# Kernel tuning notes

Measured on AMD Instinct MI355X. Metric: run time of the kernel, lower is better.

## Reference

```python
import jax, jax.numpy as jnp
import numpy as np

WS = (2, 7, 7)       # window size (d,h,w)
SS = (1, 3, 3)       # shift size
NH = 6               # num heads
EPS = 1e-5


def _layernorm(x, g, b):
    m = jnp.mean(x, axis=-1, keepdims=True)
    v = jnp.mean((x - m) ** 2, axis=-1, keepdims=True)
    return (x - m) * jax.lax.rsqrt(v + EPS) * g + b


def _window_partition(x, ws):
    # x: (B, D, H, W, C) -> (B*nW, N, C)
    B, D, H, W, C = x.shape
    x = x.reshape(B, D // ws[0], ws[0], H // ws[1], ws[1], W // ws[2], ws[2], C)
    x = x.transpose(0, 1, 3, 5, 2, 4, 6, 7)
    return x.reshape(-1, ws[0] * ws[1] * ws[2], C)


def _window_reverse(w, ws, B, D, H, W):
    # w: (B*nW, N, C) -> (B, D, H, W, C)
    C = w.shape[-1]
    x = w.reshape(B, D // ws[0], H // ws[1], W // ws[2], ws[0], ws[1], ws[2], C)
    x = x.transpose(0, 1, 4, 2, 5, 3, 6, 7)
    return x.reshape(B, D, H, W, C)


def _rel_pos_index(ws):
    coords = np.stack(np.meshgrid(np.arange(ws[0]), np.arange(ws[1]), np.arange(ws[2]), indexing='ij'))
    cf = coords.reshape(3, -1)                      # (3, N)
    rel = cf[:, :, None] - cf[:, None, :]           # (3, N, N)
    rel = rel.transpose(1, 2, 0).copy()             # (N, N, 3)
    rel[..., 0] += ws[0] - 1
    rel[..., 1] += ws[1] - 1
    rel[..., 2] += ws[2] - 1
    rel[..., 0] *= (2 * ws[1] - 1) * (2 * ws[2] - 1)
    rel[..., 1] *= 2 * ws[2] - 1
    return rel.sum(-1)                              # (N, N) int


def _compute_mask(Dp, Hp, Wp, ws, ss):
    img = np.zeros((1, Dp, Hp, Wp, 1), np.float32)
    cnt = 0
    for d in (slice(-ws[0]), slice(-ws[0], -ss[0]), slice(-ss[0], None)):
        for h in (slice(-ws[1]), slice(-ws[1], -ss[1]), slice(-ss[1], None)):
            for w in (slice(-ws[2]), slice(-ws[2], -ss[2]), slice(-ss[2], None)):
                img[:, d, h, w, :] = cnt
                cnt += 1
    mw = np.asarray(_window_partition(jnp.asarray(img), ws)).squeeze(-1)  # (nW, N)
    am = mw[:, None, :] - mw[:, :, None]
    return np.where(am != 0, -100.0, 0.0).astype(np.float32)


def setup_inputs() -> dict:
    key = jax.random.key(0)
    ks = jax.random.split(key, 8)
    B, D, H, W, C = 4, 8, 56, 56, 192
    hid = 4 * C
    tbl = (2 * WS[0] - 1) * (2 * WS[1] - 1) * (2 * WS[2] - 1)
    s = 0.02
    return {
        'x': jax.random.normal(ks[0], (B, D, H, W, C), jnp.float32),
        'mask_matrix': jnp.asarray(_compute_mask(D, H, W, WS, SS)),
        'norm1_g': jnp.ones((C,), jnp.float32),
        'norm1_b': jnp.zeros((C,), jnp.float32),
        'qkv_w': jax.random.normal(ks[1], (3 * C, C), jnp.float32) * s,
        'qkv_b': jnp.zeros((3 * C,), jnp.float32),
        'rpb_table': jax.random.normal(ks[2], (tbl, NH), jnp.float32) * s,
        'proj_w': jax.random.normal(ks[3], (C, C), jnp.float32) * s,
        'proj_b': jnp.zeros((C,), jnp.float32),
        'norm2_g': jnp.ones((C,), jnp.float32),
        'norm2_b': jnp.zeros((C,), jnp.float32),
        'fc1_w': jax.random.normal(ks[4], (hid, C), jnp.float32) * s,
        'fc1_b': jnp.zeros((hid,), jnp.float32),
        'fc2_w': jax.random.normal(ks[5], (C, hid), jnp.float32) * s,
        'fc2_b': jnp.zeros((C,), jnp.float32),
    }


def reference(x, mask_matrix, norm1_g, norm1_b, qkv_w, qkv_b, rpb_table,
              proj_w, proj_b, norm2_g, norm2_b, fc1_w, fc1_b, fc2_w, fc2_b):
    B, D, H, W, C = x.shape
    hd = C // NH
    scale = hd ** -0.5
    N = WS[0] * WS[1] * WS[2]
    rpi = _rel_pos_index(WS)  # constant (N, N)

    shortcut = x
    h = _layernorm(x, norm1_g, norm1_b)
    # cyclic shift (dims divisible by window, no padding needed)
    sx = jnp.roll(h, (-SS[0], -SS[1], -SS[2]), axis=(1, 2, 3))
    xw = _window_partition(sx, WS)                      # (B_, N, C)
    B_ = xw.shape[0]

    qkv = (xw @ qkv_w.T + qkv_b).reshape(B_, N, 3, NH, hd).transpose(2, 0, 3, 1, 4)
    q, k, v = qkv[0] * scale, qkv[1], qkv[2]            # (B_, NH, N, hd)
    attn = jnp.einsum('bhnd,bhmd->bhnm', q, k)          # (B_, NH, N, N)

    bias = rpb_table[rpi.reshape(-1)].reshape(N, N, NH).transpose(2, 0, 1)
    attn = attn + bias[None]

    nW = mask_matrix.shape[0]
    attn = attn.reshape(B_ // nW, nW, NH, N, N) + mask_matrix[None, :, None]
    attn = jax.nn.softmax(attn.reshape(B_, NH, N, N), axis=-1)

    out = jnp.einsum('bhnm,bhmd->bhnd', attn, v).swapaxes(1, 2).reshape(B_, N, C)
    out = out @ proj_w.T + proj_b

    sx = _window_reverse(out, WS, B, D, H, W)
    x1 = jnp.roll(sx, (SS[0], SS[1], SS[2]), axis=(1, 2, 3))

    x = shortcut + x1
    h2 = _layernorm(x, norm2_g, norm2_b)
    h2 = jax.nn.gelu(h2 @ fc1_w.T + fc1_b, approximate=False) @ fc2_w.T + fc2_b
    return x + h2
```

## Files before the change

kernel.cpp:

```cpp
#include <hip/hip_runtime.h>
#include <math.h>

typedef short short8 __attribute__((ext_vector_type(8)));
typedef __bf16 bf16x8 __attribute__((ext_vector_type(8)));
typedef float floatx4 __attribute__((ext_vector_type(4)));
typedef float f32x4 __attribute__((ext_vector_type(4)));
typedef unsigned short ushort;
typedef unsigned int uint;

#define NTOK 100352
#define CCH 192
#define NWIN 1024
#define NSEQ 98
#define NSEQP 112
#define NHEAD 6
#define HD 32
#define VSTR 136
#define PSTR 40

typedef const __attribute__((address_space(1))) uint guint_t;
typedef __attribute__((address_space(3))) uint luint_t;

__device__ __forceinline__ float bf2f(ushort u) {
    union { uint i; float f; } x; x.i = ((uint)u) << 16; return x.f;
}
__device__ __forceinline__ ushort f2bf(float f) {
    uint u = __float_as_uint(f);
    uint r = (u + 0x7FFFu + ((u >> 16) & 1u)) >> 16;
    return (ushort)r;
}
__device__ __forceinline__ uint pack2bf(float a, float b) {
    return (uint)f2bf(a) | ((uint)f2bf(b) << 16);
}
__device__ __forceinline__ float ldT(const void* p, size_t i, bool bf) {
    return bf ? bf2f(((const ushort*)p)[i]) : ((const float*)p)[i];
}

__global__ void detect_kernel(const uint* __restrict__ n1g, uint* __restrict__ flag) {
    if (threadIdx.x == 0) flag[0] = (n1g[0] == 0x3F800000u) ? 0u : 1u;
}

__global__ __launch_bounds__(256) void prepw_kernel(
    const void* __restrict__ src, ushort* __restrict__ dst,
    int K, const uint* __restrict__ flagp, int total)
{
    const bool bf = (*flagp != 0u);
    int e = blockIdx.x * 256 + threadIdx.x;
    if (e >= total) return;
    int j = e / K, kk = e - j * K;
    int nt = j >> 6, r = j & 63;
    int ktc = kk >> 5, c = kk & 31;
    int ci = nt * 6 + ktc;
    int byteoff = (ci << 12) + (((r << 6) + (c << 1)) ^ ((r & 7) << 4));
    *(ushort*)((char*)dst + byteoff) = f2bf(ldT(src, e, bf));
}

__global__ __launch_bounds__(256) void prepwf_kernel(
    const void* __restrict__ w1, const void* __restrict__ w2,
    const void* __restrict__ g2, ushort* __restrict__ dst,
    const uint* __restrict__ flagp)
{
    const bool bf = (*flagp != 0u);
    int e = blockIdx.x * 256 + threadIdx.x;
    if (e >= 294912) return;
    int ci, r, c; float vv;
    if (e < 147456) {
        int j = e / 192, kk = e - j * 192;
        ci = (j >> 6) * 12 + (kk >> 5);
        r = j & 63; c = kk & 31;
        vv = ldT(w1, e, bf) * ldT(g2, kk, bf);
    } else {
        int e2 = e - 147456;
        int j = e2 / 768, kk = e2 - j * 768;
        ci = (kk >> 6) * 12 + 6 + (j >> 6) * 2 + ((kk >> 5) & 1);
        r = j & 63; c = kk & 31;
        vv = ldT(w2, e2, bf);
    }
    int byteoff = (ci << 12) + (((r << 6) + (c << 1)) ^ ((r & 7) << 4));
    *(ushort*)((char*)dst + byteoff) = f2bf(vv);
}

__global__ __launch_bounds__(256) void prepmisc_kernel(
    const void* qkvb, const void* projb, const void* fc2b,
    const void* fc1b, const void* fc1w, const void* g2, const void* b2,
    float* __restrict__ FB, const uint* __restrict__ flagp)
{
    const bool bf = (*flagp != 0u);
    int j = blockIdx.x * 256 + threadIdx.x;
    if (j >= 768) return;
    if (j < 576) FB[j] = ldT(qkvb, j, bf);
    if (j < 192) { FB[576 + j] = ldT(projb, j, bf); FB[768 + j] = ldT(fc2b, j, bf); }
    float c1 = 0.f, c2 = 0.f;
    for (int kk = 0; kk < 192; ++kk) {
        float w = ldT(fc1w, (size_t)j * 192 + kk, bf);
        c1 = fmaf(w, ldT(g2, kk, bf), c1);
        c2 = fmaf(w, ldT(b2, kk, bf), c2);
    }
    FB[1728 + j] = c1;
    FB[960 + j]  = c2 + ldT(fc1b, j, bf);
}

__global__ __launch_bounds__(256) void prepTB_kernel(
    const void* __restrict__ rpb, const void* __restrict__ mask,
    float* __restrict__ TB, const uint* __restrict__ flagp)
{
    const bool bf = (*flagp != 0u);
    int i = blockIdx.x * 256 + threadIdx.x;
    if (i >= 8 * NHEAD * 7 * NSEQP * 16) return;
    int ky16 = i & 15; int t1 = i >> 4;
    int qy = t1 % NSEQP; int t2 = t1 / NSEQP;
    int kt = t2 % 7; int t3 = t2 / 7;
    int head = t3 % NHEAD; int combo = t3 / NHEAD;
    int ky = kt * 16 + ky16;
    int kcl = ky < 97 ? ky : 97, qcl = qy < 97 ? qy : 97;
    int md = kcl / 49, mr = kcl % 49; int mh = mr / 7, mw = mr % 7;
    int nd = qcl / 49, nr = qcl % 49; int nh = nr / 7, nw = nr % 7;
    int idx = (nd - md) * 169 + (nh - mh) * 13 + (nw - mw) + 253;
    float b = ldT(rpb, (size_t)idx * NHEAD + head, bf);
    int wrem = ((combo & 4) ? (3 << 6) : 0) | ((combo & 2) ? (7 << 3) : 0) | ((combo & 1) ? 7 : 0);
    float m = ldT(mask, (size_t)wrem * (NSEQ * NSEQ) + (size_t)kcl * NSEQ + qcl, bf);
    TB[i] = b + m;
}

__global__ __launch_bounds__(256) void ln1_kernel(
    const void* __restrict__ x, const void* __restrict__ g,
    const void* __restrict__ b, ushort* __restrict__ xw,
    const uint* __restrict__ flagp)
{
    const bool bf = (*flagp != 0u);
    int tid = blockIdx.x * 4 + (threadIdx.x >> 6);
    int lane = threadIdx.x & 63;
    int wi = tid / NSEQ, n = tid % NSEQ;
    int bb = wi >> 8; int rem = wi & 255;
    int wd = rem >> 6; int wh = (rem >> 3) & 7; int ww = rem & 7;
    int dz = n / 49; int r2 = n % 49; int hy = r2 / 7; int wx = r2 % 7;
    int dd = wd * 2 + dz, hh = wh * 7 + hy, w2 = ww * 7 + wx;
    int dsrc = (dd + 1) & 7;
    int hsrc = hh + 3; if (hsrc >= 56) hsrc -= 56;
    int wsrc = w2 + 3; if (wsrc >= 56) wsrc -= 56;
    size_t base = ((size_t)((bb * 8 + dsrc) * 56 + hsrc) * 56 + wsrc) * CCH;
    float v0 = ldT(x, base + lane, bf);
    float v1 = ldT(x, base + lane + 64, bf);
    float v2 = ldT(x, base + lane + 128, bf);
    float s = v0 + v1 + v2;
    float ss = v0 * v0 + v1 * v1 + v2 * v2;
    for (int o = 32; o > 0; o >>= 1) { s += __shfl_xor(s, o, 64); ss += __shfl_xor(ss, o, 64); }
    float mean = s * (1.f / 192.f);
    float var = ss * (1.f / 192.f) - mean * mean;
    float rstd = rsqrtf(var + 1e-5f);
    ushort* dst = xw + (size_t)tid * CCH;
    dst[lane]       = f2bf((v0 - mean) * rstd * ldT(g, lane, bf)       + ldT(b, lane, bf));
    dst[lane + 64]  = f2bf((v1 - mean) * rstd * ldT(g, lane + 64, bf)  + ldT(b, lane + 64, bf));
    dst[lane + 128] = f2bf((v2 - mean) * rstd * ldT(g, lane + 128, bf) + ldT(b, lane + 128, bf));
}

#define KSTEP(CI, AKP, ACC) do {                                                    \
    const int ci_ = (CI);                                                           \
    if (ci_ + 1 < TOT) {                                                            \
        const ushort* s_ = WB + ((size_t)(ci_ + 1) << 11) + (t << 3);               \
        ushort* d_ = (ushort*)Bs + (((ci_ + 1) & 1) << 11) + (wave << 9);           \
        __builtin_amdgcn_global_load_lds((guint_t*)s_, (luint_t*)d_, 16, 0, 0);     \
        asm volatile("s_waitcnt vmcnt(1) lgkmcnt(0)" ::: "memory");                 \
    } else {                                                                        \
        asm volatile("s_waitcnt vmcnt(0) lgkmcnt(0)" ::: "memory");                 \
    }                                                                               \
    __builtin_amdgcn_s_barrier();                                                   \
    __builtin_amdgcn_sched_barrier(0);                                              \
    {                                                                               \
        const char* bb_ = (const char*)Bs + ((ci_ & 1) << 12);                      \
        const ushort* ak_ = (AKP);                                                  \
        bf16x8 a0_ = __builtin_bit_cast(bf16x8, *(const short8*)(ak_ + rowA));      \
        bf16x8 a1_ = __builtin_bit_cast(bf16x8, *(const short8*)(ak_ + rowA + 640));\
        bf16x8 b0_ = __builtin_bit_cast(bf16x8, *(const short8*)(bb_ + bOff0));     \
        bf16x8 b1_ = __builtin_bit_cast(bf16x8, *(const short8*)(bb_ + bOff0 + 1024));\
        ACC[0][0] = __builtin_amdgcn_mfma_f32_16x16x32_bf16(a0_, b0_, ACC[0][0], 0, 0, 0); \
        ACC[0][1] = __builtin_amdgcn_mfma_f32_16x16x32_bf16(a0_, b1_, ACC[0][1], 0, 0, 0); \
        ACC[1][0] = __builtin_amdgcn_mfma_f32_16x16x32_bf16(a1_, b0_, ACC[1][0], 0, 0, 0); \
        ACC[1][1] = __builtin_amdgcn_mfma_f32_16x16x32_bf16(a1_, b1_, ACC[1][1], 0, 0, 0); \
    }                                                                               \
    __builtin_amdgcn_sched_barrier(0);                                              \
    __builtin_amdgcn_s_barrier();                                                   \
} while (0)

template <int MODE>
__global__ __launch_bounds__(256, 4) void gemm_kernel(
    const ushort* __restrict__ Abf, const ushort* __restrict__ WB,
    const float* __restrict__ bias,
    ushort* __restrict__ o0, ushort* __restrict__ o1, ushort* __restrict__ o2,
    const void* __restrict__ xorig, ushort* __restrict__ xnewB,
    float* __restrict__ statsOut, const uint* __restrict__ flagp)
{
    constexpr int NT  = (MODE == 0) ? 9 : 3;
    constexpr int TOT = NT * 6;
    const bool bf = (*flagp != 0u);
    __shared__ alignas(16) ushort As[15360];
    __shared__ alignas(16) ushort Bs[4096];
    const int t = threadIdx.x, wave = t >> 6, lane = t & 63;
    const int q = lane >> 4, l15 = lane & 15;
    const int wr = wave >> 1, wc = wave & 1;
    const int m0 = blockIdx.x * 64;
    const int rowA  = (wr * 32 + l15) * 40 + q * 8;
    const int bOff0 = ((wc * 32 + l15) * 64 + q * 16) ^ ((l15 & 7) << 4);
    const int sr = t >> 2, scg = (t & 3) * 8;

    {
        const ushort* s0 = WB + (t << 3);
        ushort* d0 = (ushort*)Bs + (wave << 9);
        __builtin_amdgcn_global_load_lds((guint_t*)s0, (luint_t*)d0, 16, 0, 0);
    }
    {
        const ushort* arow = Abf + (size_t)(m0 + sr) * 192 + scg;
        ushort* dA = As + sr * 40 + scg;
#pragma unroll
        for (int kt = 0; kt < 6; ++kt)
            *(short8*)(dA + kt * 2560) = *(const short8*)(arow + kt * 32);
    }

    float ssum[2][4] = {{0.f,0.f,0.f,0.f},{0.f,0.f,0.f,0.f}};
    float ssq[2][4]  = {{0.f,0.f,0.f,0.f},{0.f,0.f,0.f,0.f}};
    for (int nt = 0; nt < NT; ++nt) {
        floatx4 acc[2][2];
#pragma unroll
        for (int mi = 0; mi < 2; ++mi)
#pragma unroll
            for (int ni = 0; ni < 2; ++ni) acc[mi][ni] = (floatx4){0.f, 0.f, 0.f, 0.f};
#pragma unroll
        for (int kt = 0; kt < 6; ++kt) KSTEP(nt * 6 + kt, As + kt * 2560, acc);

        if constexpr (MODE == 0) {
#pragma unroll
            for (int mi = 0; mi < 2; ++mi)
#pragma unroll
            for (int rr = 0; rr < 4; ++rr) {
                int m = m0 + wr * 32 + mi * 16 + q * 4 + rr;
                int wi2 = m / NSEQ, nn = m - wi2 * NSEQ;
#pragma unroll
                for (int ni = 0; ni < 2; ++ni) {
                    int j = nt * 64 + wc * 32 + ni * 16 + l15;
                    float val = acc[mi][ni][rr] + bias[j];
                    int which = j / 192, remj = j - which * 192;
                    int head = remj >> 5, dd = remj & 31;
                    size_t off = (((size_t)(wi2 * NHEAD + head)) * NSEQ + nn) * HD + dd;
                    if (which == 0)      o0[off] = f2bf(val * 0.17677669529663687f);
                    else if (which == 1) o1[off] = f2bf(val);
                    else                 o2[off] = f2bf(val);
                }
            }
        } else {
#pragma unroll
            for (int mi = 0; mi < 2; ++mi)
#pragma unroll
            for (int rr = 0; rr < 4; ++rr) {
                int m = m0 + wr * 32 + mi * 16 + q * 4 + rr;
                int wi2 = m / NSEQ, nn = m - wi2 * NSEQ;
                int bb2 = wi2 >> 8; int remw = wi2 & 255;
                int wd = remw >> 6, wh = (remw >> 3) & 7, ww = remw & 7;
                int dz = nn / 49; int r2 = nn - dz * 49; int hy = r2 / 7, wx = r2 - hy * 7;
                int dd2 = wd * 2 + dz, hh = wh * 7 + hy, w2 = ww * 7 + wx;
                int df = (dd2 + 1) & 7;
                int hf = hh + 3; if (hf >= 56) hf -= 56;
                int wf = w2 + 3; if (wf >= 56) wf -= 56;
                size_t rowb = ((size_t)((bb2 * 8 + df) * 56 + hf) * 56 + wf) * CCH;
#pragma unroll
                for (int ni = 0; ni < 2; ++ni) {
                    int j = nt * 64 + wc * 32 + ni * 16 + l15;
                    size_t idx = rowb + j;
                    float res = ldT(xorig, idx, bf) + acc[mi][ni][rr] + bias[j];
                    xnewB[idx] = f2bf(res);
                    ssum[mi][rr] += res;
                    ssq[mi][rr]  += res * res;
                }
            }
        }
    }
    if constexpr (MODE == 1) {
#pragma unroll
        for (int mi = 0; mi < 2; ++mi)
#pragma unroll
        for (int rr = 0; rr < 4; ++rr) {
#pragma unroll
            for (int off = 1; off <= 8; off <<= 1) {
                ssum[mi][rr] += __shfl_xor(ssum[mi][rr], off, 64);
                ssq[mi][rr]  += __shfl_xor(ssq[mi][rr], off, 64);
            }
        }
        __syncthreads();
        float* sm = (float*)Bs;
        if (wc == 0 && l15 == 0) {
#pragma unroll
            for (int mi = 0; mi < 2; ++mi)
#pragma unroll
            for (int rr = 0; rr < 4; ++rr) {
                int tl = wr * 32 + mi * 16 + q * 4 + rr;
                sm[2 * tl] = ssum[mi][rr];
                sm[2 * tl + 1] = ssq[mi][rr];
            }
        }
        __syncthreads();
        if (wc == 1 && l15 == 0) {
#pragma unroll
            for (int mi = 0; mi < 2; ++mi)
#pragma unroll
            for (int rr = 0; rr < 4; ++rr) {
                int tl = wr * 32 + mi * 16 + q * 4 + rr;
                float s  = sm[2 * tl] + ssum[mi][rr];
                float s2 = sm[2 * tl + 1] + ssq[mi][rr];
                float mean = s * (1.f / 192.f);
                float var = s2 * (1.f / 192.f) - mean * mean;
                int m = m0 + tl;
                int wi2 = m / NSEQ, nn = m - wi2 * NSEQ;
                int bb2 = wi2 >> 8; int remw = wi2 & 255;
                int wd = remw >> 6, wh = (remw >> 3) & 7, ww = remw & 7;
                int dz = nn / 49; int r2 = nn - dz * 49; int hy = r2 / 7, wx = r2 - hy * 7;
                int dd2 = wd * 2 + dz, hh = wh * 7 + hy, w2 = ww * 7 + wx;
                int df = (dd2 + 1) & 7;
                int hf = hh + 3; if (hf >= 56) hf -= 56;
                int wf = w2 + 3; if (wf >= 56) wf -= 56;
                int spat = ((bb2 * 8 + df) * 56 + hf) * 56 + wf;
                statsOut[2 * spat]     = mean;
                statsOut[2 * spat + 1] = rsqrtf(var + 1e-5f);
            }
        }
    }
}

__global__ __launch_bounds__(256, 3) void fc_kernel(
    const ushort* __restrict__ trunk, const float* __restrict__ stats,
    const ushort* __restrict__ WB, const float* __restrict__ cb,
    const float* __restrict__ c1p, const float* __restrict__ f2b,
    void* __restrict__ outAny, const uint* __restrict__ flagp)
{
    constexpr int TOT = 144;
    const bool bf = (*flagp != 0u);
    __shared__ alignas(16) ushort As[15360];
    __shared__ alignas(16) ushort Hs[5120];
    __shared__ alignas(16) ushort Bs[4096];
    const int t = threadIdx.x, wave = t >> 6, lane = t & 63;
    const int q = lane >> 4, l15 = lane & 15;
    const int wr = wave >> 1, wc = wave & 1;
    const int m0 = blockIdx.x * 64;
    const int rowA  = (wr * 32 + l15) * 40 + q * 8;
    const int bOff0 = ((wc * 32 + l15) * 64 + q * 16) ^ ((l15 & 7) << 4);
    const int sr = t >> 2, scg = (t & 3) * 8;

    {
        const ushort* s0 = WB + (t << 3);
        ushort* d0 = (ushort*)Bs + (wave << 9);
        __builtin_amdgcn_global_load_lds((guint_t*)s0, (luint_t*)d0, 16, 0, 0);
    }
    {
        const ushort* arow = trunk + (size_t)(m0 + sr) * 192 + scg;
        ushort* dA = As + sr * 40 + scg;
#pragma unroll
        for (int kt = 0; kt < 6; ++kt)
            *(short8*)(dA + kt * 2560) = *(const short8*)(arow + kt * 32);
    }
    float rstd_[2][4], mrs_[2][4];
#pragma unroll
    for (int mi = 0; mi < 2; ++mi)
#pragma unroll
    for (int rr = 0; rr < 4; ++rr) {
        int m = m0 + wr * 32 + mi * 16 + q * 4 + rr;
        float mean = stats[2 * m], rs = stats[2 * m + 1];
        rstd_[mi][rr] = rs; mrs_[mi][rr] = mean * rs;
    }

    floatx4 f2a[3][2][2];
#pragma unroll
    for (int n3 = 0; n3 < 3; ++n3)
#pragma unroll
        for (int mi = 0; mi < 2; ++mi)
#pragma unroll
            for (int ni = 0; ni < 2; ++ni) f2a[n3][mi][ni] = (floatx4){0.f, 0.f, 0.f, 0.f};

    for (int ht = 0; ht < 12; ++ht) {
        floatx4 a1[2][2];
#pragma unroll
        for (int mi = 0; mi < 2; ++mi)
#pragma unroll
            for (int ni = 0; ni < 2; ++ni) a1[mi][ni] = (floatx4){0.f, 0.f, 0.f, 0.f};
#pragma unroll
        for (int kt = 0; kt < 6; ++kt) KSTEP(ht * 12 + kt, As + kt * 2560, a1);

        float c1v0 = c1p[ht * 64 + wc * 32 + l15];
        float c1v1 = c1p[ht * 64 + wc * 32 + 16 + l15];
        float cbv0 = cb[ht * 64 + wc * 32 + l15];
        float cbv1 = cb[ht * 64 + wc * 32 + 16 + l15];
        ushort* hp = Hs + wc * 2560;
#pragma unroll
        for (int mi = 0; mi < 2; ++mi)
#pragma unroll
        for (int ni = 0; ni < 2; ++ni)
#pragma unroll
        for (int rr = 0; rr < 4; ++rr) {
            float val = a1[mi][ni][rr] * rstd_[mi][rr]
                      - mrs_[mi][rr] * (ni ? c1v1 : c1v0) + (ni ? cbv1 : cbv0);
            float gl = 0.5f * val * (1.0f + erff(val * 0.70710678118654752f));
            hp[(wr * 32 + mi * 16 + q * 4 + rr) * 40 + ni * 16 + l15] = f2bf(gl);
        }
        __syncthreads();
#pragma unroll
        for (int nt3 = 0; nt3 < 3; ++nt3)
#pragma unroll
            for (int kt2 = 0; kt2 < 2; ++kt2)
                KSTEP(ht * 12 + 6 + nt3 * 2 + kt2, Hs + kt2 * 2560, f2a[nt3]);
        __syncthreads();
    }

#pragma unroll
    for (int nt3 = 0; nt3 < 3; ++nt3)
#pragma unroll
    for (int mi = 0; mi < 2; ++mi)
#pragma unroll
    for (int rr = 0; rr < 4; ++rr) {
        int mrow = wr * 32 + mi * 16 + q * 4 + rr;
        int m = m0 + mrow;
#pragma unroll
        for (int ni = 0; ni < 2; ++ni) {
            int j = nt3 * 64 + wc * 32 + ni * 16 + l15;
            float res = f2a[nt3][mi][ni][rr] + f2b[j]
                      + bf2f(As[(j >> 5) * 2560 + mrow * 40 + (j & 31)]);
            size_t oi = (size_t)m * CCH + j;
            if (bf) ((ushort*)outAny)[oi] = f2bf(res);
            else    ((float*)outAny)[oi]  = res;
        }
    }
}

__global__ __launch_bounds__(128, 4) void attn_kernel(
    const ushort* __restrict__ qg, const ushort* __restrict__ kg,
    const ushort* __restrict__ vg, const float* __restrict__ TB,
    ushort* __restrict__ out)
{
    __shared__ alignas(16) ushort Vt[32 * VSTR];
    __shared__ alignas(16) ushort Ps[NSEQP * PSTR];
    const int blk = blockIdx.x;
    const int wi = blk / NHEAD, head = blk - wi * NHEAD;
    const int tid = threadIdx.x;
    const int wave = tid >> 6, lane = tid & 63;
    const int q = lane >> 4, l15 = lane & 15;
    const size_t base = (size_t)blk * (NSEQ * HD);

    {
        const uint* vp = (const uint*)(vg + base);
        for (int i = 0; i < 13; ++i) {
            int e2 = i * 128 + tid;
            if (e2 < 1568) {
                uint w = vp[e2];
                int key = e2 >> 4, d = (e2 & 15) * 2;
                Vt[d * VSTR + key]       = (ushort)(w & 0xFFFFu);
                Vt[(d + 1) * VSTR + key] = (ushort)(w >> 16);
            }
        }
        for (int i = 0; i < 8; ++i) {
            int idx = i * 128 + tid;
            if (idx < 960) {
                int d = idx / 30, key = 98 + (idx - d * 30);
                Vt[d * VSTR + key] = 0;
            }
        }
    }

    const int ntBeg = wave ? 4 : 0;
    const int NTW   = wave ? 3 : 4;

    bf16x8 qf[4];
#pragma unroll
    for (int i = 0; i < 4; ++i)
        if (i < NTW)
            qf[i] = __builtin_bit_cast(bf16x8,
                *(const short8*)(qg + base + (size_t)((ntBeg + i) * 16 + l15) * HD + q * 8));

    const int wrem = wi & 255;
    const int combo = (((wrem >> 6) == 3) ? 4 : 0) | ((((wrem >> 3) & 7) == 7) ? 2 : 0)
                    | (((wrem & 7) == 7) ? 1 : 0);
    const float* bt = TB + (size_t)(combo * NHEAD + head) * (7 * NSEQP * 16);

    floatx4 oacc[2][4];
#pragma unroll
    for (int dt = 0; dt < 2; ++dt)
#pragma unroll
        for (int i = 0; i < 4; ++i) oacc[dt][i] = (floatx4){0.f, 0.f, 0.f, 0.f};
    float rs[4] = {0.f, 0.f, 0.f, 0.f};

    __syncthreads();

    for (int ks = 0; ks < 4; ++ks) {
#pragma unroll
        for (int h = 0; h < 2; ++h) {
            const int kt = ks * 2 + h;
            if (kt < 7) {
                bf16x8 kfr = __builtin_bit_cast(bf16x8,
                    *(const short8*)(kg + base + (size_t)(kt * 16 + l15) * HD + q * 8));
                floatx4 st[4];
#pragma unroll
                for (int i = 0; i < 4; ++i)
                    if (i < NTW)
                        st[i] = __builtin_amdgcn_mfma_f32_16x16x32_bf16(
                            kfr, qf[i], (floatx4){0.f, 0.f, 0.f, 0.f}, 0, 0, 0);
#pragma unroll
                for (int i = 0; i < 4; ++i) {
                    if (i >= NTW) continue;
                    const int qy = (ntBeg + i) * 16 + l15;
                    f32x4 bv = *(const f32x4*)(bt + ((size_t)kt * NSEQP + qy) * 16 + q * 4);
                    float p[4];
#pragma unroll
                    for (int r = 0; r < 4; ++r) {
                        float pe = __expf(st[i][r] + bv[r]);
                        if (kt == 6 && (q * 4 + r) >= 2) pe = 0.f;
                        p[r] = pe;
                    }
                    rs[i] += (p[0] + p[1]) + (p[2] + p[3]);
                    uint* pr = (uint*)(Ps + (size_t)qy * PSTR + h * 16 + q * 4);
                    pr[0] = pack2bf(p[0], p[1]);
                    pr[1] = pack2bf(p[2], p[3]);
                }
            } else {
#pragma unroll
                for (int i = 0; i < 4; ++i) {
                    if (i >= NTW) continue;
                    uint* z = (uint*)(Ps + (size_t)((ntBeg + i) * 16 + l15) * PSTR + 16 + q * 4);
                    z[0] = 0u; z[1] = 0u;
                }
            }
        }
        bf16x8 va[2];
#pragma unroll
        for (int dt = 0; dt < 2; ++dt)
            va[dt] = __builtin_bit_cast(bf16x8,
                *(const short8*)(Vt + (size_t)(dt * 16 + l15) * VSTR + ks * 32 + q * 8));
#pragma unroll
        for (int i = 0; i < 4; ++i) {
            if (i >= NTW) continue;
            bf16x8 pb = __builtin_bit_cast(bf16x8,
                *(const short8*)(Ps + (size_t)((ntBeg + i) * 16 + l15) * PSTR + q * 8));
            oacc[0][i] = __builtin_amdgcn_mfma_f32_16x16x32_bf16(va[0], pb, oacc[0][i], 0, 0, 0);
            oacc[1][i] = __builtin_amdgcn_mfma_f32_16x16x32_bf16(va[1], pb, oacc[1][i], 0, 0, 0);
        }
    }

#pragma unroll
    for (int i = 0; i < 4; ++i) {
        float r = rs[i];
        r += __shfl_xor(r, 16, 64);
        r += __shfl_xor(r, 32, 64);
        rs[i] = 1.f / r;
    }
#pragma unroll
    for (int i = 0; i < 4; ++i) {
        if (i >= NTW) continue;
        const int nt = ntBeg + i;
        const int qy = nt * 16 + l15;
        if (nt == 6 && l15 >= 2) continue;
        ushort* op = out + ((size_t)wi * NSEQ + qy) * CCH + head * HD;
        const float inv = rs[i];
#pragma unroll
        for (int dt = 0; dt < 2; ++dt) {
            const int d0 = dt * 16 + q * 4;
            *(uint*)(op + d0)     = pack2bf(oacc[dt][i][0] * inv, oacc[dt][i][1] * inv);
            *(uint*)(op + d0 + 2) = pack2bf(oacc[dt][i][2] * inv, oacc[dt][i][3] * inv);
        }
    }
}

extern "C" void kernel_launch(void* const* d_in, const int* in_sizes, int n_in,
                              void* d_out, int out_size, void* d_ws, size_t ws_size,
                              hipStream_t stream)
{
    const void* x     = d_in[0];
    const void* mask  = d_in[1];
    const void* n1g   = d_in[2];
    const void* n1b   = d_in[3];
    const void* qkvw  = d_in[4];
    const void* qkvb  = d_in[5];
    const void* rpb   = d_in[6];
    const void* projw = d_in[7];
    const void* projb = d_in[8];
    const void* n2g   = d_in[9];
    const void* n2b   = d_in[10];
    const void* fc1w  = d_in[11];
    const void* fc1b  = d_in[12];
    const void* fc2w  = d_in[13];
    const void* fc2b  = d_in[14];

    char* ws = (char*)d_ws;
    const size_t SZB = (size_t)NTOK * CCH * 2;
    ushort* xw     = (ushort*)(ws);
    ushort* q      = (ushort*)(ws + SZB);
    ushort* k      = (ushort*)(ws + 2 * SZB);
    ushort* v      = (ushort*)(ws + 3 * SZB);
    ushort* xnewB  = (ushort*)(ws + 4 * SZB);
    float*  TB     = (float*)(ws + 5 * SZB);
    float*  stats  = (float*)(ws + 6 * SZB);
    uint*   flag   = (uint*)(ws + 6 * SZB + 802816);
    char*   blob   = ws + 6 * SZB + 802816 + 256;
    ushort* WQ = (ushort*)(blob);
    ushort* WP = (ushort*)(blob + 221184);
    ushort* WF = (ushort*)(blob + 294912);
    float*  FB = (float*)(blob + 884736);

    detect_kernel<<<1, 64, 0, stream>>>((const uint*)n1g, flag);
    prepmisc_kernel<<<3, 256, 0, stream>>>(qkvb, projb, fc2b, fc1b, fc1w, n2g, n2b, FB, flag);
    prepTB_kernel<<<2352, 256, 0, stream>>>(rpb, mask, TB, flag);
    prepw_kernel<<<432, 256, 0, stream>>>(qkvw, WQ, 192, flag, 110592);
    prepw_kernel<<<144, 256, 0, stream>>>(projw, WP, 192, flag, 36864);
    prepwf_kernel<<<1152, 256, 0, stream>>>(fc1w, fc2w, n2g, WF, flag);
    ln1_kernel<<<NTOK / 4, 256, 0, stream>>>(x, n1g, n1b, xw, flag);
    gemm_kernel<0><<<NTOK / 64, 256, 0, stream>>>(
        xw, WQ, FB, q, k, v, nullptr, nullptr, nullptr, flag);
    attn_kernel<<<NWIN * NHEAD, 128, 0, stream>>>(q, k, v, TB, xw);
    gemm_kernel<1><<<NTOK / 64, 256, 0, stream>>>(
        xw, WP, FB + 576, nullptr, nullptr, nullptr, x, xnewB, stats, flag);
    fc_kernel<<<NTOK / 64, 256, 0, stream>>>(
        xnewB, stats, WF, FB + 960, FB + 1728, FB + 768, d_out, flag);
}
```

Measured before the change: 648.7 us.

## Double-buffer weight tiles in pairs and hold A fragments in registers in MLP kernel

The fused MLP kernel now streams weight tiles two at a time into a double-buffered LDS region, prefetching the next pair while the current pair feeds the MFMAs. This halves the number of barrier/wait points per k-step. It also loads the normalized input A fragments into registers once instead of rereading LDS every hidden tile. The cost is more LDS for B and more VGPRs for the cached fragments, which could lower occupancy under launch_bounds(256,3).

```diff
diff --git a/kernel.cpp b/kernel.cpp
--- a/kernel.cpp
+++ b/kernel.cpp
@@ -324,17 +324,37 @@
     }
 }
 
+#define PAIR_SYNC(GP) do {                                                          \
+    const int gp_ = (GP);                                                           \
+    if (gp_ + 1 < 72) {                                                             \
+        const ushort* s0_ = WB + ((size_t)(2 * gp_ + 2) << 11) + (t << 3);          \
+        const ushort* s1_ = WB + ((size_t)(2 * gp_ + 3) << 11) + (t << 3);          \
+        ushort* d0_ = (ushort*)Bs + ((gp_ + 1) & 1) * 4096 + (wave << 9);           \
+        ushort* d1_ = (ushort*)Bs + ((gp_ + 1) & 1) * 4096 + 2048 + (wave << 9);    \
+        __builtin_amdgcn_global_load_lds((guint_t*)s0_, (luint_t*)d0_, 16, 0, 0);   \
+        __builtin_amdgcn_global_load_lds((guint_t*)s1_, (luint_t*)d1_, 16, 0, 0);   \
+        asm volatile("s_waitcnt vmcnt(2) lgkmcnt(0)" ::: "memory");                 \
+    } else {                                                                        \
+        asm volatile("s_waitcnt vmcnt(0) lgkmcnt(0)" ::: "memory");                 \
+    }                                                                               \
+    __builtin_amdgcn_s_barrier();                                                   \
+    __builtin_amdgcn_sched_barrier(0);                                              \
+} while (0)
+#define PAIR_END() do {                                                             \
+    __builtin_amdgcn_sched_barrier(0);                                              \
+    __builtin_amdgcn_s_barrier();                                                   \
+} while (0)
+
 __global__ __launch_bounds__(256, 3) void fc_kernel(
     const ushort* __restrict__ trunk, const float* __restrict__ stats,
     const ushort* __restrict__ WB, const float* __restrict__ cb,
     const float* __restrict__ c1p, const float* __restrict__ f2b,
     void* __restrict__ outAny, const uint* __restrict__ flagp)
 {
-    constexpr int TOT = 144;
     const bool bf = (*flagp != 0u);
     __shared__ alignas(16) ushort As[15360];
     __shared__ alignas(16) ushort Hs[5120];
-    __shared__ alignas(16) ushort Bs[4096];
+    __shared__ alignas(16) ushort Bs[8192];
     const int t = threadIdx.x, wave = t >> 6, lane = t & 63;
     const int q = lane >> 4, l15 = lane & 15;
     const int wr = wave >> 1, wc = wave & 1;
@@ -345,8 +365,11 @@
 
     {
         const ushort* s0 = WB + (t << 3);
+        const ushort* s1 = WB + 2048 + (t << 3);
         ushort* d0 = (ushort*)Bs + (wave << 9);
+        ushort* d1 = (ushort*)Bs + 2048 + (wave << 9);
         __builtin_amdgcn_global_load_lds((guint_t*)s0, (luint_t*)d0, 16, 0, 0);
+        __builtin_amdgcn_global_load_lds((guint_t*)s1, (luint_t*)d1, 16, 0, 0);
     }
     {
         const ushort* arow = trunk + (size_t)(m0 + sr) * 192 + scg;
@@ -355,6 +378,16 @@
         for (int kt = 0; kt < 6; ++kt)
             *(short8*)(dA + kt * 2560) = *(const short8*)(arow + kt * 32);
     }
+    __syncthreads();
+
+    bf16x8 afr[6][2];
+#pragma unroll
+    for (int kt = 0; kt < 6; ++kt)
+#pragma unroll
+        for (int mi = 0; mi < 2; ++mi)
+            afr[kt][mi] = __builtin_bit_cast(bf16x8,
+                *(const short8*)(As + kt * 2560 + rowA + mi * 640));
+
     float rstd_[2][4], mrs_[2][4];
 #pragma unroll
     for (int mi = 0; mi < 2; ++mi)
@@ -379,8 +412,27 @@
         for (int mi = 0; mi < 2; ++mi)
 #pragma unroll
             for (int ni = 0; ni < 2; ++ni) a1[mi][ni] = (floatx4){0.f, 0.f, 0.f, 0.f};
-#pragma unroll
-        for (int kt = 0; kt < 6; ++kt) KSTEP(ht * 12 + kt, As + kt * 2560, a1);
+
+#pragma unroll
+        for (int p = 0; p < 3; ++p) {
+            const int gp = ht * 6 + p;
+            PAIR_SYNC(gp);
+            {
+                const char* sb = (const char*)Bs + (gp & 1) * 8192;
+#pragma unroll
+                for (int h2 = 0; h2 < 2; ++h2) {
+                    const int kt = 2 * p + h2;
+                    const char* bb_ = sb + h2 * 4096;
+                    bf16x8 b0_ = __builtin_bit_cast(bf16x8, *(const short8*)(bb_ + bOff0));
+                    bf16x8 b1_ = __builtin_bit_cast(bf16x8, *(const short8*)(bb_ + bOff0 + 1024));
+                    a1[0][0] = __builtin_amdgcn_mfma_f32_16x16x32_bf16(afr[kt][0], b0_, a1[0][0], 0, 0, 0);
+                    a1[0][1] = __builtin_amdgcn_mfma_f32_16x16x32_bf16(afr[kt][0], b1_, a1[0][1], 0, 0, 0);
+                    a1[1][0] = __builtin_amdgcn_mfma_f32_16x16x32_bf16(afr[kt][1], b0_, a1[1][0], 0, 0, 0);
+                    a1[1][1] = __builtin_amdgcn_mfma_f32_16x16x32_bf16(afr[kt][1], b1_, a1[1][1], 0, 0, 0);
+                }
+            }
+            PAIR_END();
+        }
 
         float c1v0 = c1p[ht * 64 + wc * 32 + l15];
         float c1v1 = c1p[ht * 64 + wc * 32 + 16 + l15];
@@ -398,13 +450,29 @@
             float gl = 0.5f * val * (1.0f + erff(val * 0.70710678118654752f));
             hp[(wr * 32 + mi * 16 + q * 4 + rr) * 40 + ni * 16 + l15] = f2bf(gl);
         }
-        __syncthreads();
-#pragma unroll
-        for (int nt3 = 0; nt3 < 3; ++nt3)
-#pragma unroll
-            for (int kt2 = 0; kt2 < 2; ++kt2)
-                KSTEP(ht * 12 + 6 + nt3 * 2 + kt2, Hs + kt2 * 2560, f2a[nt3]);
-        __syncthreads();
+
+#pragma unroll
+        for (int p = 0; p < 3; ++p) {
+            const int gp = ht * 6 + 3 + p;
+            PAIR_SYNC(gp);
+            {
+                const char* sb = (const char*)Bs + (gp & 1) * 8192;
+#pragma unroll
+                for (int kt2 = 0; kt2 < 2; ++kt2) {
+                    const ushort* hk = Hs + kt2 * 2560;
+                    bf16x8 a0_ = __builtin_bit_cast(bf16x8, *(const short8*)(hk + rowA));
+                    bf16x8 a1_ = __builtin_bit_cast(bf16x8, *(const short8*)(hk + rowA + 640));
+                    const char* bb_ = sb + kt2 * 4096;
+                    bf16x8 b0_ = __builtin_bit_cast(bf16x8, *(const short8*)(bb_ + bOff0));
+                    bf16x8 b1_ = __builtin_bit_cast(bf16x8, *(const short8*)(bb_ + bOff0 + 1024));
+                    f2a[p][0][0] = __builtin_amdgcn_mfma_f32_16x16x32_bf16(a0_, b0_, f2a[p][0][0], 0, 0, 0);
+                    f2a[p][0][1] = __builtin_amdgcn_mfma_f32_16x16x32_bf16(a0_, b1_, f2a[p][0][1], 0, 0, 0);
+                    f2a[p][1][0] = __builtin_amdgcn_mfma_f32_16x16x32_bf16(a1_, b0_, f2a[p][1][0], 0, 0, 0);
+                    f2a[p][1][1] = __builtin_amdgcn_mfma_f32_16x16x32_bf16(a1_, b1_, f2a[p][1][1], 0, 0, 0);
+                }
+            }
+            PAIR_END();
+        }
     }
 
 #pragma unroll
```

Result: faster. 628.5 us (-3.1%).
